# Kernel tuning notes

Hardware: AMD Instinct MI355X
Metric: run time of the kernel (lower is better)

The kernel has to match this reference:

```python
import jax, jax.numpy as jnp
import numpy as np

N = 1048576
INPUT_CH = 3
INPUT_CH_VIEWS = 3
HIDDEN = 64
GEO_FEAT = 15


def setup_inputs() -> dict:
    key = jax.random.key(0)
    ks = jax.random.split(key, 8)
    def w(k, out_d, in_d):
        # torch nn.Linear default init: U(-1/sqrt(in), 1/sqrt(in)), weight shape [out, in]
        bound = 1.0 / np.sqrt(in_d)
        return jax.random.uniform(k, (out_d, in_d), jnp.float32, -bound, bound)
    return {
        "x": jax.random.normal(ks[0], (N, INPUT_CH + INPUT_CH_VIEWS), jnp.float32),
        "sw0": w(ks[1], HIDDEN, INPUT_CH),
        "sw1": w(ks[2], HIDDEN, HIDDEN),
        "sw2": w(ks[3], 1 + GEO_FEAT, HIDDEN),
        "cw0": w(ks[4], HIDDEN, INPUT_CH_VIEWS + GEO_FEAT),
        "cw1": w(ks[5], HIDDEN, HIDDEN),
        "cw2": w(ks[6], HIDDEN, HIDDEN),
        "cw3": w(ks[7], 3, HIDDEN),
    }


def reference(x, sw0, sw1, sw2, cw0, cw1, cw2, cw3):
    input_pts = x[..., :INPUT_CH]          # [N, 3]
    input_views = x[..., INPUT_CH:]        # [N, 3]

    # sigma network: Linear(no bias) + ReLU (no ReLU on last layer)
    h = jax.nn.relu(input_pts @ sw0.T)     # [N, 64]
    h = jax.nn.relu(h @ sw1.T)             # [N, 64]
    h = h @ sw2.T                          # [N, 16]
    sigma = h[..., 0]                      # [N]
    geo_feat = h[..., 1:]                  # [N, 15]

    # color network
    h = jnp.concatenate([input_views, geo_feat], axis=-1)  # [N, 18]
    h = jax.nn.relu(h @ cw0.T)             # [N, 64]
    h = jax.nn.relu(h @ cw1.T)             # [N, 64]
    h = jax.nn.relu(h @ cw2.T)             # [N, 64]
    color = h @ cw3.T                      # [N, 3]

    return jnp.concatenate([color, sigma[..., None]], axis=-1)  # [N, 4]
```

## Files before the change

### kernel.cpp

```cpp
#include <hip/hip_runtime.h>
#include <stdint.h>

typedef __attribute__((ext_vector_type(8))) _Float16 half8;
typedef __attribute__((ext_vector_type(2))) __fp16 fp16x2;
typedef __attribute__((ext_vector_type(16))) float floatx16;
typedef __attribute__((ext_vector_type(2))) short s16x2;
typedef unsigned int u32;
typedef unsigned short u16;

#define TPW 8


__device__ __forceinline__ u32 pkf16(float a, float b) {
  union { fp16x2 v; u32 u; } c;
  c.v = __builtin_amdgcn_cvt_pkrtz(a, b);
  return c.u;
}

__device__ __forceinline__ u32 relu_pk(u32 t) {
  union { u32 u; s16x2 v; } c;
  c.u = t;
  s16x2 zz = {0, 0};
  c.v = __builtin_elementwise_max(c.v, zz);
  return c.u;
}

__device__ __forceinline__ u16 rtnh(float a) {
  union { _Float16 h; u16 u; } c;
  c.h = (_Float16)a;
  return c.u;
}

__device__ __forceinline__ int sigperm(int k) {
  int r = k & 15;
  int s = (r & 3) | ((r & 4) << 1) | ((r & 8) >> 1);
  return (k & ~15) | s;
}

__device__ __forceinline__ half8 packhalf(const floatx16 a, int base, bool relu) {
  union { u32 u[4]; half8 v; } r;
#pragma unroll
  for (int i = 0; i < 4; ++i) {
    u32 t = pkf16(a[base + 2 * i], a[base + 2 * i + 1]);
    r.u[i] = relu ? relu_pk(t) : t;
  }
  return r.v;
}

#define MFMA(A, B, C) __builtin_amdgcn_mfma_f32_32x32x16_f16(A, B, C, 0, 0, 0)

#define NFRAG 38

__global__ void build_pool(
    const float* __restrict__ w_s0, const float* __restrict__ w_s1,
    const float* __restrict__ w_s2, const float* __restrict__ w_c0,
    const float* __restrict__ w_c1, const float* __restrict__ w_c2,
    const float* __restrict__ w_c3, uint4* __restrict__ pool) {
  const int f = blockIdx.x;
  const int lane = threadIdx.x;
  const int m = lane & 31;
  const int kb = (lane >> 5) << 3;

  union { u16 e[8]; uint4 q; } u;
  if (f < 2) {
    const int row = f * 32 + m;
#pragma unroll
    for (int j = 0; j < 8; ++j) {
      const int k = kb + j;
      u.e[j] = (k < 3) ? rtnh(w_s0[row * 3 + k]) : (u16)0;
    }
  } else if (f < 10) {
    const int g = f - 2, rt = g >> 2, ks = g & 3;
    const int row = rt * 32 + m;
#pragma unroll
    for (int j = 0; j < 8; ++j)
      u.e[j] = rtnh(w_s1[row * 64 + sigperm(ks * 16 + kb + j)]);
  } else if (f < 14) {
    const int ks = f - 10;
    const int row = (m < 16) ? m : 0;
#pragma unroll
    for (int j = 0; j < 8; ++j) {
      u16 v = rtnh(w_s2[row * 64 + sigperm(ks * 16 + kb + j)]);
      u.e[j] = (m < 16) ? v : (u16)0;
    }
  } else if (f < 18) {
    const int g = f - 14, rt = g >> 1, ks = g & 1;
    const int row = rt * 32 + m;
#pragma unroll
    for (int j = 0; j < 8; ++j) {
      if (ks == 0) {
        const int c = sigperm(kb + j);
        u16 v = rtnh(w_c0[row * 18 + (c + 2)]);
        u.e[j] = (c == 0) ? (u16)0 : v;
      } else {
        const int kk = kb + j;
        u16 v = rtnh(w_c0[row * 18 + kk]);
        u.e[j] = (kk < 3) ? v : (u16)0;
      }
    }
  } else if (f < 26) {
    const int g = f - 18, rt = g >> 2, ks = g & 3;
    const int row = rt * 32 + m;
#pragma unroll
    for (int j = 0; j < 8; ++j)
      u.e[j] = rtnh(w_c1[row * 64 + sigperm(ks * 16 + kb + j)]);
  } else if (f < 34) {
    const int g = f - 26, rt = g >> 2, ks = g & 3;
    const int row = rt * 32 + m;
#pragma unroll
    for (int j = 0; j < 8; ++j)
      u.e[j] = rtnh(w_c2[row * 64 + sigperm(ks * 16 + kb + j)]);
  } else {
    const int ks = f - 34;
    const int row = (m < 3) ? m : 0;
#pragma unroll
    for (int j = 0; j < 8; ++j) {
      u16 v = rtnh(w_c3[row * 64 + sigperm(ks * 16 + kb + j)]);
      u.e[j] = (m < 3) ? v : (u16)0;
    }
  }
  pool[f * 64 + lane] = u.q;
}

__global__ __launch_bounds__(256, 2) void nerf_fused(
    const float* __restrict__ x, const uint4* __restrict__ pool,
    float* __restrict__ out, int npts) {
  const int lane = threadIdx.x & 63;
  const int wid = threadIdx.x >> 6;
  const int m = lane & 31;
  const int hi = lane >> 5;

#define GW(F) (*(const half8*)((const u16*)pool + (F) * 512 + lane * 8))

  const half8 W0 = GW(0),   W1 = GW(1);
  const half8 W2 = GW(2),   W3 = GW(3),   W4 = GW(4),   W5 = GW(5);
  const half8 W6 = GW(6),   W7 = GW(7),   W8 = GW(8),   W9 = GW(9);
  const half8 W10 = GW(10), W11 = GW(11), W12 = GW(12), W13 = GW(13);
  const half8 W14 = GW(14), W15 = GW(15), W16 = GW(16), W17 = GW(17);
  const half8 W18 = GW(18), W19 = GW(19), W20 = GW(20), W21 = GW(21);
  const half8 W22 = GW(22), W23 = GW(23), W24 = GW(24), W25 = GW(25);
  const half8 W26 = GW(26), W27 = GW(27), W28 = GW(28), W29 = GW(29);
  const half8 W30 = GW(30), W31 = GW(31), W32 = GW(32), W33 = GW(33);

  const int ntiles = npts >> 5;
  const int wave = blockIdx.x * 4 + wid;
  const floatx16 z = (floatx16)0.0f;

#pragma unroll 1
  for (int t = 0; t < TPW; ++t) {
    const int tile = wave * TPW + t;
    if (tile >= ntiles) break;
    const int pt = (tile << 5) | m;

    const float2* xp = (const float2*)(x + (size_t)pt * 6);
    const float2 a0 = xp[0], a1 = xp[1], a2 = xp[2];

    union { u32 u[4]; half8 v; } bx, bv;
    bx.u[0] = hi ? 0u : pkf16(a0.x, a0.y);
    bx.u[1] = hi ? 0u : pkf16(a1.x, 0.0f);
    bx.u[2] = 0u; bx.u[3] = 0u;
    bv.u[0] = hi ? 0u : pkf16(a1.y, a2.x);
    bv.u[1] = hi ? 0u : pkf16(a2.y, 0.0f);
    bv.u[2] = 0u; bv.u[3] = 0u;

    floatx16 h0, h1;
    half8 p0, p1, p2, p3, q0, q1, q2, q3;

    h0 = MFMA(W0, bx.v, z);
    h1 = MFMA(W1, bx.v, z);
    p0 = packhalf(h0, 0, true); p1 = packhalf(h0, 8, true);
    p2 = packhalf(h1, 0, true); p3 = packhalf(h1, 8, true);

    h0 = MFMA(W2, p0, z);  h1 = MFMA(W6, p0, z);
    h0 = MFMA(W3, p1, h0); h1 = MFMA(W7, p1, h1);
    h0 = MFMA(W4, p2, h0); h1 = MFMA(W8, p2, h1);
    h0 = MFMA(W5, p3, h0); h1 = MFMA(W9, p3, h1);
    q0 = packhalf(h0, 0, true); q1 = packhalf(h0, 8, true);
    q2 = packhalf(h1, 0, true); q3 = packhalf(h1, 8, true);

    h0 = MFMA(W10, q0, z);
    h0 = MFMA(W11, q1, h0);
    h0 = MFMA(W12, q2, h0);
    h0 = MFMA(W13, q3, h0);
    const float sigma = h0[0];
    const half8 bs2 = packhalf(h0, 0, false);

    h0 = MFMA(W14, bs2, z);   h1 = MFMA(W16, bs2, z);
    h0 = MFMA(W15, bv.v, h0); h1 = MFMA(W17, bv.v, h1);
    p0 = packhalf(h0, 0, true); p1 = packhalf(h0, 8, true);
    p2 = packhalf(h1, 0, true); p3 = packhalf(h1, 8, true);

    const half8 C0 = GW(34), C1 = GW(35), C2 = GW(36), C3 = GW(37);

    h0 = MFMA(W18, p0, z);  h1 = MFMA(W22, p0, z);
    h0 = MFMA(W19, p1, h0); h1 = MFMA(W23, p1, h1);
    h0 = MFMA(W20, p2, h0); h1 = MFMA(W24, p2, h1);
    h0 = MFMA(W21, p3, h0); h1 = MFMA(W25, p3, h1);
    q0 = packhalf(h0, 0, true); q1 = packhalf(h0, 8, true);
    q2 = packhalf(h1, 0, true); q3 = packhalf(h1, 8, true);

    h0 = MFMA(W26, q0, z);  h1 = MFMA(W30, q0, z);
    h0 = MFMA(W27, q1, h0); h1 = MFMA(W31, q1, h1);
    h0 = MFMA(W28, q2, h0); h1 = MFMA(W32, q2, h1);
    h0 = MFMA(W29, q3, h0); h1 = MFMA(W33, q3, h1);
    p0 = packhalf(h0, 0, true); p1 = packhalf(h0, 8, true);
    p2 = packhalf(h1, 0, true); p3 = packhalf(h1, 8, true);

    h0 = MFMA(C0, p0, z);
    h0 = MFMA(C1, p1, h0);
    h0 = MFMA(C2, p2, h0);
    h0 = MFMA(C3, p3, h0);

    if (lane < 32) {
      float4 o;
      o.x = h0[0]; o.y = h0[1]; o.z = h0[2]; o.w = sigma;
      *(float4*)(out + (size_t)pt * 4) = o;
    }
  }
#undef GW
}

extern "C" void kernel_launch(void* const* d_in, const int* in_sizes, int n_in,
                              void* d_out, int out_size, void* d_ws, size_t ws_size,
                              hipStream_t stream) {
  const float* x = (const float*)d_in[0];
  const float* sw0 = (const float*)d_in[1];
  const float* sw1 = (const float*)d_in[2];
  const float* sw2 = (const float*)d_in[3];
  const float* cw0 = (const float*)d_in[4];
  const float* cw1 = (const float*)d_in[5];
  const float* cw2 = (const float*)d_in[6];
  const float* cw3 = (const float*)d_in[7];
  float* out = (float*)d_out;
  uint4* pool = (uint4*)d_ws;

  const int npts = in_sizes[0] / 6;
  const int ntiles = npts >> 5;
  const int blocks = (ntiles + 4 * TPW - 1) / (4 * TPW);

  build_pool<<<NFRAG, 64, 0, stream>>>(sw0, sw1, sw2, cw0, cw1, cw2, cw3, pool);
  nerf_fused<<<blocks, 256, 0, stream>>>(x, pool, out, npts);
}
```

Before: 115.1 us.

## Stage MLP weights in LDS and software-pipeline sigma/color stages across tiles

Weights are copied once per block into shared memory and read from there per MFMA, instead of being held in registers after a global load. The per-tile loop is restructured so the sigma half of tile t+1 is issued after the color half of tile t, giving the scheduler independent work to interleave. The branch on lane < 32 around the store is replaced by sending the upper lanes' store to a dump buffer. This adds LDS traffic and drops any partial tail tile (a wave returns early if it has fewer than TPW full tiles).

```diff
diff --git a/kernel.cpp b/kernel.cpp
--- a/kernel.cpp
+++ b/kernel.cpp
@@ -122,102 +122,112 @@
   pool[f * 64 + lane] = u.q;
 }
 
+__device__ __forceinline__ half8 ldw(const u16* wl, int F, int lane) {
+  return *(const half8*)(wl + F * 512 + lane * 8);
+}
+
+__device__ __forceinline__ void sigma_half(
+    const u16* __restrict__ wl, const float* __restrict__ x,
+    int tile, int lane, int m, int hi,
+    half8& P0, half8& P1, half8& P2, half8& P3, float& bsig, int& bpt) {
+  const floatx16 z = (floatx16)0.0f;
+  const int pt = (tile << 5) | m;
+  const float2* xp = (const float2*)(x + (size_t)pt * 6);
+  const float2 a0 = xp[0], a1 = xp[1], a2 = xp[2];
+
+  union { u32 u[4]; half8 v; } bx, bv;
+  bx.u[0] = hi ? 0u : pkf16(a0.x, a0.y);
+  bx.u[1] = hi ? 0u : pkf16(a1.x, 0.0f);
+  bx.u[2] = 0u; bx.u[3] = 0u;
+  bv.u[0] = hi ? 0u : pkf16(a1.y, a2.x);
+  bv.u[1] = hi ? 0u : pkf16(a2.y, 0.0f);
+  bv.u[2] = 0u; bv.u[3] = 0u;
+
+  floatx16 h0, h1;
+  h0 = MFMA(ldw(wl, 0, lane), bx.v, z);
+  h1 = MFMA(ldw(wl, 1, lane), bx.v, z);
+  half8 p0 = packhalf(h0, 0, true), p1 = packhalf(h0, 8, true);
+  half8 p2 = packhalf(h1, 0, true), p3 = packhalf(h1, 8, true);
+  h0 = MFMA(ldw(wl, 2, lane), p0, z);  h1 = MFMA(ldw(wl, 6, lane), p0, z);
+  h0 = MFMA(ldw(wl, 3, lane), p1, h0); h1 = MFMA(ldw(wl, 7, lane), p1, h1);
+  h0 = MFMA(ldw(wl, 4, lane), p2, h0); h1 = MFMA(ldw(wl, 8, lane), p2, h1);
+  h0 = MFMA(ldw(wl, 5, lane), p3, h0); h1 = MFMA(ldw(wl, 9, lane), p3, h1);
+  half8 q0 = packhalf(h0, 0, true), q1 = packhalf(h0, 8, true);
+  half8 q2 = packhalf(h1, 0, true), q3 = packhalf(h1, 8, true);
+  h0 = MFMA(ldw(wl, 10, lane), q0, z);
+  h0 = MFMA(ldw(wl, 11, lane), q1, h0);
+  h0 = MFMA(ldw(wl, 12, lane), q2, h0);
+  h0 = MFMA(ldw(wl, 13, lane), q3, h0);
+  bsig = h0[0];
+  const half8 bs2 = packhalf(h0, 0, false);
+  h0 = MFMA(ldw(wl, 14, lane), bs2, z);   h1 = MFMA(ldw(wl, 16, lane), bs2, z);
+  h0 = MFMA(ldw(wl, 15, lane), bv.v, h0); h1 = MFMA(ldw(wl, 17, lane), bv.v, h1);
+  P0 = packhalf(h0, 0, true); P1 = packhalf(h0, 8, true);
+  P2 = packhalf(h1, 0, true); P3 = packhalf(h1, 8, true);
+  bpt = pt;
+}
+
+__device__ __forceinline__ void color_half(
+    const u16* __restrict__ wl, float* __restrict__ out,
+    float* __restrict__ dump, int lane,
+    half8 P0, half8 P1, half8 P2, half8 P3, float bsig, int bpt) {
+  const floatx16 z = (floatx16)0.0f;
+  floatx16 h0, h1;
+  h0 = MFMA(ldw(wl, 18, lane), P0, z);  h1 = MFMA(ldw(wl, 22, lane), P0, z);
+  h0 = MFMA(ldw(wl, 19, lane), P1, h0); h1 = MFMA(ldw(wl, 23, lane), P1, h1);
+  h0 = MFMA(ldw(wl, 20, lane), P2, h0); h1 = MFMA(ldw(wl, 24, lane), P2, h1);
+  h0 = MFMA(ldw(wl, 21, lane), P3, h0); h1 = MFMA(ldw(wl, 25, lane), P3, h1);
+  half8 q0 = packhalf(h0, 0, true), q1 = packhalf(h0, 8, true);
+  half8 q2 = packhalf(h1, 0, true), q3 = packhalf(h1, 8, true);
+  h0 = MFMA(ldw(wl, 26, lane), q0, z);  h1 = MFMA(ldw(wl, 30, lane), q0, z);
+  h0 = MFMA(ldw(wl, 27, lane), q1, h0); h1 = MFMA(ldw(wl, 31, lane), q1, h1);
+  h0 = MFMA(ldw(wl, 28, lane), q2, h0); h1 = MFMA(ldw(wl, 32, lane), q2, h1);
+  h0 = MFMA(ldw(wl, 29, lane), q3, h0); h1 = MFMA(ldw(wl, 33, lane), q3, h1);
+  half8 r0 = packhalf(h0, 0, true), r1 = packhalf(h0, 8, true);
+  half8 r2 = packhalf(h1, 0, true), r3 = packhalf(h1, 8, true);
+  h0 = MFMA(ldw(wl, 34, lane), r0, z);
+  h0 = MFMA(ldw(wl, 35, lane), r1, h0);
+  h0 = MFMA(ldw(wl, 36, lane), r2, h0);
+  h0 = MFMA(ldw(wl, 37, lane), r3, h0);
+
+  float4 o;
+  o.x = h0[0]; o.y = h0[1]; o.z = h0[2]; o.w = bsig;
+  float* dst = (lane < 32) ? (out + (size_t)bpt * 4) : (dump + (lane & 31) * 4);
+  *(float4*)dst = o;
+}
+
 __global__ __launch_bounds__(256, 2) void nerf_fused(
     const float* __restrict__ x, const uint4* __restrict__ pool,
-    float* __restrict__ out, int npts) {
+    float* __restrict__ out, float* __restrict__ dump, int npts) {
+  __shared__ __align__(16) u16 wl[NFRAG * 512];
+
+  {
+    uint4* lp = (uint4*)wl;
+    for (int i = threadIdx.x; i < NFRAG * 64; i += 256) lp[i] = pool[i];
+  }
+  __syncthreads();
+
   const int lane = threadIdx.x & 63;
   const int wid = threadIdx.x >> 6;
   const int m = lane & 31;
   const int hi = lane >> 5;
 
-#define GW(F) (*(const half8*)((const u16*)pool + (F) * 512 + lane * 8))
-
-  const half8 W0 = GW(0),   W1 = GW(1);
-  const half8 W2 = GW(2),   W3 = GW(3),   W4 = GW(4),   W5 = GW(5);
-  const half8 W6 = GW(6),   W7 = GW(7),   W8 = GW(8),   W9 = GW(9);
-  const half8 W10 = GW(10), W11 = GW(11), W12 = GW(12), W13 = GW(13);
-  const half8 W14 = GW(14), W15 = GW(15), W16 = GW(16), W17 = GW(17);
-  const half8 W18 = GW(18), W19 = GW(19), W20 = GW(20), W21 = GW(21);
-  const half8 W22 = GW(22), W23 = GW(23), W24 = GW(24), W25 = GW(25);
-  const half8 W26 = GW(26), W27 = GW(27), W28 = GW(28), W29 = GW(29);
-  const half8 W30 = GW(30), W31 = GW(31), W32 = GW(32), W33 = GW(33);
-
   const int ntiles = npts >> 5;
   const int wave = blockIdx.x * 4 + wid;
-  const floatx16 z = (floatx16)0.0f;
-
+  const int base = wave * TPW;
+  if (base + TPW > ntiles) return;
+
+  half8 P0, P1, P2, P3;
+  float bsig;
+  int bpt;
+
+  sigma_half(wl, x, base, lane, m, hi, P0, P1, P2, P3, bsig, bpt);
 #pragma unroll 1
-  for (int t = 0; t < TPW; ++t) {
-    const int tile = wave * TPW + t;
-    if (tile >= ntiles) break;
-    const int pt = (tile << 5) | m;
-
-    const float2* xp = (const float2*)(x + (size_t)pt * 6);
-    const float2 a0 = xp[0], a1 = xp[1], a2 = xp[2];
-
-    union { u32 u[4]; half8 v; } bx, bv;
-    bx.u[0] = hi ? 0u : pkf16(a0.x, a0.y);
-    bx.u[1] = hi ? 0u : pkf16(a1.x, 0.0f);
-    bx.u[2] = 0u; bx.u[3] = 0u;
-    bv.u[0] = hi ? 0u : pkf16(a1.y, a2.x);
-    bv.u[1] = hi ? 0u : pkf16(a2.y, 0.0f);
-    bv.u[2] = 0u; bv.u[3] = 0u;
-
-    floatx16 h0, h1;
-    half8 p0, p1, p2, p3, q0, q1, q2, q3;
-
-    h0 = MFMA(W0, bx.v, z);
-    h1 = MFMA(W1, bx.v, z);
-    p0 = packhalf(h0, 0, true); p1 = packhalf(h0, 8, true);
-    p2 = packhalf(h1, 0, true); p3 = packhalf(h1, 8, true);
-
-    h0 = MFMA(W2, p0, z);  h1 = MFMA(W6, p0, z);
-    h0 = MFMA(W3, p1, h0); h1 = MFMA(W7, p1, h1);
-    h0 = MFMA(W4, p2, h0); h1 = MFMA(W8, p2, h1);
-    h0 = MFMA(W5, p3, h0); h1 = MFMA(W9, p3, h1);
-    q0 = packhalf(h0, 0, true); q1 = packhalf(h0, 8, true);
-    q2 = packhalf(h1, 0, true); q3 = packhalf(h1, 8, true);
-
-    h0 = MFMA(W10, q0, z);
-    h0 = MFMA(W11, q1, h0);
-    h0 = MFMA(W12, q2, h0);
-    h0 = MFMA(W13, q3, h0);
-    const float sigma = h0[0];
-    const half8 bs2 = packhalf(h0, 0, false);
-
-    h0 = MFMA(W14, bs2, z);   h1 = MFMA(W16, bs2, z);
-    h0 = MFMA(W15, bv.v, h0); h1 = MFMA(W17, bv.v, h1);
-    p0 = packhalf(h0, 0, true); p1 = packhalf(h0, 8, true);
-    p2 = packhalf(h1, 0, true); p3 = packhalf(h1, 8, true);
-
-    const half8 C0 = GW(34), C1 = GW(35), C2 = GW(36), C3 = GW(37);
-
-    h0 = MFMA(W18, p0, z);  h1 = MFMA(W22, p0, z);
-    h0 = MFMA(W19, p1, h0); h1 = MFMA(W23, p1, h1);
-    h0 = MFMA(W20, p2, h0); h1 = MFMA(W24, p2, h1);
-    h0 = MFMA(W21, p3, h0); h1 = MFMA(W25, p3, h1);
-    q0 = packhalf(h0, 0, true); q1 = packhalf(h0, 8, true);
-    q2 = packhalf(h1, 0, true); q3 = packhalf(h1, 8, true);
-
-    h0 = MFMA(W26, q0, z);  h1 = MFMA(W30, q0, z);
-    h0 = MFMA(W27, q1, h0); h1 = MFMA(W31, q1, h1);
-    h0 = MFMA(W28, q2, h0); h1 = MFMA(W32, q2, h1);
-    h0 = MFMA(W29, q3, h0); h1 = MFMA(W33, q3, h1);
-    p0 = packhalf(h0, 0, true); p1 = packhalf(h0, 8, true);
-    p2 = packhalf(h1, 0, true); p3 = packhalf(h1, 8, true);
-
-    h0 = MFMA(C0, p0, z);
-    h0 = MFMA(C1, p1, h0);
-    h0 = MFMA(C2, p2, h0);
-    h0 = MFMA(C3, p3, h0);
-
-    if (lane < 32) {
-      float4 o;
-      o.x = h0[0]; o.y = h0[1]; o.z = h0[2]; o.w = sigma;
-      *(float4*)(out + (size_t)pt * 4) = o;
-    }
-  }
-#undef GW
+  for (int t = 1; t < TPW; ++t) {
+    color_half(wl, out, dump, lane, P0, P1, P2, P3, bsig, bpt);
+    sigma_half(wl, x, base + t, lane, m, hi, P0, P1, P2, P3, bsig, bpt);
+  }
+  color_half(wl, out, dump, lane, P0, P1, P2, P3, bsig, bpt);
 }
 
 extern "C" void kernel_launch(void* const* d_in, const int* in_sizes, int n_in,
@@ -233,11 +243,12 @@
   const float* cw3 = (const float*)d_in[7];
   float* out = (float*)d_out;
   uint4* pool = (uint4*)d_ws;
+  float* dump = (float*)((char*)d_ws + NFRAG * 1024);
 
   const int npts = in_sizes[0] / 6;
   const int ntiles = npts >> 5;
   const int blocks = (ntiles + 4 * TPW - 1) / (4 * TPW);
 
   build_pool<<<NFRAG, 64, 0, stream>>>(sw0, sw1, sw2, cw0, cw1, cw2, cw3, pool);
-  nerf_fused<<<blocks, 256, 0, stream>>>(x, pool, out, npts);
-}
+  nerf_fused<<<blocks, 256, 0, stream>>>(x, pool, out, dump, npts);
+}
```

Result: no change. 113.4 us (-1.5%).
